# Optimization experiments

Hardware: AMD Instinct MI355X
Metric: run time of the kernel (lower is better)

The kernel has to match this reference:

```python
import jax, jax.numpy as jnp
import numpy as np

B, N, DIN, DOUT = 8, 2048, 512, 512

def setup_inputs() -> dict:
    key = jax.random.key(0)
    kx, ka, kw, kb, kattn = jax.random.split(key, 5)
    x = jax.random.normal(kx, (B, N, DIN), dtype=jnp.float32)
    adjacency_matrix = jax.random.randint(ka, (B, N, N), 0, 2, dtype=jnp.int32)
    # nn.Linear(in,out): weight [out,in], bias [out]
    lim_w = float(np.sqrt(1.0 / DIN))
    W = jax.random.uniform(kw, (DOUT, DIN), minval=-lim_w, maxval=lim_w, dtype=jnp.float32)
    b = jax.random.uniform(kb, (DOUT,), minval=-lim_w, maxval=lim_w, dtype=jnp.float32)
    # xavier_uniform for attn [out,out]
    lim_a = float(np.sqrt(6.0 / (DOUT + DOUT)))
    attn = jax.random.uniform(kattn, (DOUT, DOUT), minval=-lim_a, maxval=lim_a, dtype=jnp.float32)
    return {"x": x, "adjacency_matrix": adjacency_matrix, "W": W, "b": b, "attn": attn}

def reference(x, adjacency_matrix, W, b, attn):
    h = jnp.einsum('bni,oi->bno', x, W) + b                 # [B,N,DOUT]
    ha = jnp.einsum('bmi,ij->bmj', h, attn)                  # h @ attn
    scores = jnp.einsum('bmj,bnj->bmn', ha, h)               # bilinear pairwise scores
    scores = jnp.where(adjacency_matrix == 0, -jnp.inf, scores)
    attn_weights = jax.nn.softmax(scores, axis=-1)           # adjacency-masked softmax
    x_out = jnp.einsum('bmn,bnd->bmd', attn_weights, h)      # weighted aggregation
    return jax.nn.elu(x_out)
```

## Files before the change

kernel.cpp:

```cpp
#include <hip/hip_runtime.h>
#include <cstdint>
#include <cstddef>

typedef unsigned short u16;
using f16x8 = __attribute__((ext_vector_type(8))) _Float16;
using f32x4 = __attribute__((ext_vector_type(4))) float;
using u16x4 = __attribute__((ext_vector_type(4))) unsigned short;

__device__ __forceinline__ u16 f2h(float f) {
  union { _Float16 h; u16 u; } c;
  c.h = (_Float16)f;
  return c.u;
}

__device__ __forceinline__ void gl_lds16(const void* g, void* lds) {
  __builtin_amdgcn_global_load_lds(
      (const __attribute__((address_space(1))) void*)(uintptr_t)g,
      (__attribute__((address_space(3))) void*)(uint32_t)(uintptr_t)lds,
      16, 0, 0);
}

template <int N> __device__ __forceinline__ void vmcnt_wait() {
  if constexpr (N == 0)      asm volatile("s_waitcnt vmcnt(0)" ::: "memory");
  else if constexpr (N == 3) asm volatile("s_waitcnt vmcnt(3)" ::: "memory");
  else if constexpr (N == 4) asm volatile("s_waitcnt vmcnt(4)" ::: "memory");
  else static_assert(N == 0, "unsupported vmcnt literal");
}

__device__ __forceinline__ void block_sync() {
  asm volatile("" ::: "memory");
  __builtin_amdgcn_s_barrier();
  asm volatile("" ::: "memory");
}

template <int ROWS>
__device__ __forceinline__ void stage32(const u16* g, int ldk, u16* lds, int t) {
#pragma unroll
  for (int i = 0; i < ROWS / 128; ++i) {
    const int s   = i * 512 + t;
    const int row = s >> 2;
    const int gc  = (s & 3) ^ ((s >> 3) & 3);
    gl_lds16(g + (size_t)row * ldk + gc * 8,
             lds + (size_t)(i * 512 + (t & ~63)) * 8);
  }
}

template <int NF>
__device__ __forceinline__ void compute_tile32(
    const u16* pA, const u16* pB, f32x4 (&acc)[8][NF],
    int wm, int wn, int lm, int cq)
{
  f16x8 bf[NF];
#pragma unroll
  for (int nf = 0; nf < NF; ++nf)
    bf[nf] = *(const f16x8*)(pB + (wn + nf * 16 + lm) * 32 + cq * 8);
#pragma unroll
  for (int mf = 0; mf < 8; ++mf) {
    f16x8 a0 = *(const f16x8*)(pA + (wm + mf * 16 + lm) * 32 + cq * 8);
#pragma unroll
    for (int nf = 0; nf < NF; ++nf)
      acc[mf][nf] = __builtin_amdgcn_mfma_f32_16x16x32_f16(a0, bf[nf], acc[mf][nf], 0, 0, 0);
  }
}

template <int BN, int MODE>
__global__ __launch_bounds__(512, 2) void gemm32(
    const u16* __restrict__ A, const u16* __restrict__ Bt,
    void* __restrict__ Cv, const float* __restrict__ bias,
    int M, int Ncols, int K,
    long long strideA, long long strideB, long long strideC)
{
  constexpr int NF  = BN / 64;
  constexpr int LPT = 2 + BN / 128;

  __shared__ __align__(16) u16 sA0[256 * 32];
  __shared__ __align__(16) u16 sA1[256 * 32];
  __shared__ __align__(16) u16 sA2[256 * 32];
  __shared__ __align__(16) u16 sA3[256 * 32];
  __shared__ __align__(16) u16 sB0[BN * 32];
  __shared__ __align__(16) u16 sB1[BN * 32];
  __shared__ __align__(16) u16 sB2[BN * 32];
  __shared__ __align__(16) u16 sB3[BN * 32];

  const int bz = blockIdx.z;
  A  += (size_t)bz * strideA;
  Bt += (size_t)bz * strideB;

  const int m0 = blockIdx.y * 256;
  const int n0 = blockIdx.x * BN;
  const int t    = threadIdx.x;
  const int lane = t & 63;
  const int wave = t >> 6;
  const int wm   = (wave >> 2) * 128;
  const int wn   = (wave & 3) * (BN / 4);
  const int lm   = lane & 15;
  const int quad = lane >> 4;
  const int cq   = quad ^ ((lm >> 1) & 3);

  f32x4 acc[8][NF];
#pragma unroll
  for (int i = 0; i < 8; ++i)
#pragma unroll
    for (int j = 0; j < NF; ++j) acc[i][j] = f32x4{0.f, 0.f, 0.f, 0.f};

  const u16* Ag = A + (size_t)m0 * K;
  const u16* Bg = Bt + (size_t)n0 * K;

  const int nk = K >> 5;

  stage32<256>(Ag,      K, sA0, t);  stage32<BN>(Bg,      K, sB0, t);
  stage32<256>(Ag + 32, K, sA1, t);  stage32<BN>(Bg + 32, K, sB1, t);

  for (int kt = 0; kt < nk - 4; kt += 4) {
    vmcnt_wait<LPT>(); block_sync();
    stage32<256>(Ag + (size_t)(kt + 2) * 32, K, sA2, t);
    stage32<BN >(Bg + (size_t)(kt + 2) * 32, K, sB2, t);
    compute_tile32<NF>(sA0, sB0, acc, wm, wn, lm, cq);

    vmcnt_wait<LPT>(); block_sync();
    stage32<256>(Ag + (size_t)(kt + 3) * 32, K, sA3, t);
    stage32<BN >(Bg + (size_t)(kt + 3) * 32, K, sB3, t);
    compute_tile32<NF>(sA1, sB1, acc, wm, wn, lm, cq);

    vmcnt_wait<LPT>(); block_sync();
    stage32<256>(Ag + (size_t)(kt + 4) * 32, K, sA0, t);
    stage32<BN >(Bg + (size_t)(kt + 4) * 32, K, sB0, t);
    compute_tile32<NF>(sA2, sB2, acc, wm, wn, lm, cq);

    vmcnt_wait<LPT>(); block_sync();
    stage32<256>(Ag + (size_t)(kt + 5) * 32, K, sA1, t);
    stage32<BN >(Bg + (size_t)(kt + 5) * 32, K, sB1, t);
    compute_tile32<NF>(sA3, sB3, acc, wm, wn, lm, cq);
  }

  vmcnt_wait<LPT>(); block_sync();
  stage32<256>(Ag + (size_t)(nk - 2) * 32, K, sA2, t);
  stage32<BN >(Bg + (size_t)(nk - 2) * 32, K, sB2, t);
  compute_tile32<NF>(sA0, sB0, acc, wm, wn, lm, cq);

  vmcnt_wait<LPT>(); block_sync();
  stage32<256>(Ag + (size_t)(nk - 1) * 32, K, sA3, t);
  stage32<BN >(Bg + (size_t)(nk - 1) * 32, K, sB3, t);
  compute_tile32<NF>(sA1, sB1, acc, wm, wn, lm, cq);

  vmcnt_wait<LPT>(); block_sync();
  compute_tile32<NF>(sA2, sB2, acc, wm, wn, lm, cq);

  vmcnt_wait<0>(); block_sync();
  compute_tile32<NF>(sA3, sB3, acc, wm, wn, lm, cq);

  if (MODE == 0) {
    u16* C = (u16*)Cv + (size_t)bz * strideC;
#pragma unroll
    for (int nf = 0; nf < NF; ++nf) {
      const int col = n0 + wn + nf * 16 + lm;
      const float bv = bias ? bias[col] : 0.f;
#pragma unroll
      for (int mf = 0; mf < 8; ++mf)
#pragma unroll
        for (int r = 0; r < 4; ++r) {
          const int row = m0 + wm + mf * 16 + quad * 4 + r;
          C[(size_t)row * Ncols + col] = f2h(acc[mf][nf][r] + bv);
        }
    }
  } else {
    float* C = (float*)Cv + (size_t)bz * strideC;
#pragma unroll
    for (int nf = 0; nf < NF; ++nf) {
      const int col = n0 + wn + nf * 16 + lm;
#pragma unroll
      for (int mf = 0; mf < 8; ++mf)
#pragma unroll
        for (int r = 0; r < 4; ++r) {
          const int row = m0 + wm + mf * 16 + quad * 4 + r;
          float v = acc[mf][nf][r];
          if (MODE == 2) v = v > 0.f ? v : expm1f(v);
          C[(size_t)row * Ncols + col] = v;
        }
    }
  }
}

__global__ __launch_bounds__(256) void masked_softmax(
    const float* __restrict__ S, const int* __restrict__ adj, u16* __restrict__ P)
{
  const size_t row = blockIdx.x;
  const float* s = S + row * 2048;
  const int*   a = adj + row * 2048;
  u16*         p = P + row * 2048;
  const int t = threadIdx.x;

  float v[8];
#pragma unroll
  for (int i = 0; i < 2; ++i) {
    float4 sv = ((const float4*)s)[t + i * 256];
    int4   av = ((const int4*)a)[t + i * 256];
    v[i * 4 + 0] = av.x ? sv.x : -1e30f;
    v[i * 4 + 1] = av.y ? sv.y : -1e30f;
    v[i * 4 + 2] = av.z ? sv.z : -1e30f;
    v[i * 4 + 3] = av.w ? sv.w : -1e30f;
  }
  float mx = v[0];
#pragma unroll
  for (int i = 1; i < 8; ++i) mx = fmaxf(mx, v[i]);
#pragma unroll
  for (int o = 32; o > 0; o >>= 1) mx = fmaxf(mx, __shfl_xor(mx, o));
  __shared__ float red[4];
  if ((t & 63) == 0) red[t >> 6] = mx;
  __syncthreads();
  mx = fmaxf(fmaxf(red[0], red[1]), fmaxf(red[2], red[3]));
  __syncthreads();

  float e[8]; float sum = 0.f;
#pragma unroll
  for (int i = 0; i < 8; ++i) { e[i] = __expf(v[i] - mx); sum += e[i]; }
#pragma unroll
  for (int o = 32; o > 0; o >>= 1) sum += __shfl_xor(sum, o);
  if ((t & 63) == 0) red[t >> 6] = sum;
  __syncthreads();
  sum = red[0] + red[1] + red[2] + red[3];
  const float inv = 1.f / sum;

#pragma unroll
  for (int i = 0; i < 2; ++i) {
    u16x4 o4;
    o4[0] = f2h(e[i * 4 + 0] * inv);
    o4[1] = f2h(e[i * 4 + 1] * inv);
    o4[2] = f2h(e[i * 4 + 2] * inv);
    o4[3] = f2h(e[i * 4 + 3] * inv);
    ((u16x4*)p)[t + i * 256] = o4;
  }
}

__global__ __launch_bounds__(256) void transpose_u16(
    const u16* __restrict__ in, u16* __restrict__ outp, int R, int C)
{
  __shared__ u16 tile[64][65];
  const size_t base = (size_t)blockIdx.z * R * C;
  const int r0 = blockIdx.y * 64, c0 = blockIdx.x * 64;
  const int t = threadIdx.x;
  const int c = t & 63, rr = t >> 6;
#pragma unroll
  for (int i = 0; i < 16; ++i) {
    const int r = rr + i * 4;
    tile[r][c] = in[base + (size_t)(r0 + r) * C + c0 + c];
  }
  __syncthreads();
  const int rp = t & 63, cc = t >> 6;
#pragma unroll
  for (int i = 0; i < 16; ++i) {
    const int cq2 = cc + i * 4;
    outp[base + (size_t)(c0 + cq2) * R + r0 + rp] = tile[rp][cq2];
  }
}

__global__ __launch_bounds__(256) void cvt_f32_f16(
    const float* __restrict__ in, u16* __restrict__ outp, int n4)
{
  const int i = blockIdx.x * 256 + threadIdx.x;
  if (i >= n4) return;
  float4 v = ((const float4*)in)[i];
  u16x4 o; o[0] = f2h(v.x); o[1] = f2h(v.y); o[2] = f2h(v.z); o[3] = f2h(v.w);
  ((u16x4*)outp)[i] = o;
}

__global__ __launch_bounds__(256) void transpose_cvt(
    const float* __restrict__ in, u16* __restrict__ outp, int R, int C)
{
  const int idx = blockIdx.x * 256 + threadIdx.x;
  const int i = idx / C, j = idx % C;
  outp[(size_t)j * R + i] = f2h(in[idx]);
}

extern "C" void kernel_launch(void* const* d_in, const int* in_sizes, int n_in,
                              void* d_out, int out_size, void* d_ws, size_t ws_size,
                              hipStream_t stream) {
  (void)in_sizes; (void)n_in; (void)out_size;
  const float* x    = (const float*)d_in[0];
  const int*   adj  = (const int*)d_in[1];
  const float* W    = (const float*)d_in[2];
  const float* bvec = (const float*)d_in[3];
  const float* attn = (const float*)d_in[4];
  float* out = (float*)d_out;

  constexpr int B = 8, N = 2048, D = 512;
  constexpr size_t MN = (size_t)B * N;

  char* ws = (char*)d_ws;
  size_t off = 0;
  auto take = [&](size_t bytes) -> char* {
    char* p = ws + off;
    off += (bytes + 255) & ~(size_t)255;
    return p;
  };
  u16* xh   = (u16*)take(MN * D * 2);
  u16* Wh   = (u16*)take((size_t)D * D * 2);
  u16* attT = (u16*)take((size_t)D * D * 2);
  u16* h    = (u16*)take(MN * D * 2);
  u16* hT   = (u16*)take(MN * D * 2);
  u16* ha   = (u16*)take(MN * D * 2);

  auto al = [](size_t b) { return (b + 255) & ~(size_t)255; };
  const size_t szSf = al((size_t)B * N * N * 4), szPf = al((size_t)B * N * N * 2);
  const size_t szSb = al((size_t)N * N * 4),     szPb = al((size_t)N * N * 2);
  const bool full  = ws_size >= off + szSf + szPf;
  const bool ok_pb = ws_size >= off + szSb + szPb;
  if (!full && !ok_pb) return;

  cvt_f32_f16<<<dim3((unsigned)(MN * D / 4 / 256)), 256, 0, stream>>>(x, xh, (int)(MN * D / 4));
  cvt_f32_f16<<<dim3(D * D / 4 / 256), 256, 0, stream>>>(W, Wh, D * D / 4);
  transpose_cvt<<<dim3(D * D / 256), 256, 0, stream>>>(attn, attT, D, D);

  gemm32<128, 0><<<dim3(D / 128, MN / 256, 1), 512, 0, stream>>>(
      xh, Wh, h, bvec, (int)MN, D, D, 0, 0, 0);
  transpose_u16<<<dim3(D / 64, N / 64, B), 256, 0, stream>>>(h, hT, N, D);
  gemm32<128, 0><<<dim3(D / 128, MN / 256, 1), 512, 0, stream>>>(
      h, attT, ha, nullptr, (int)MN, D, D, 0, 0, 0);

  if (full) {
    float* S = (float*)take(szSf);
    u16*   P = (u16*)take(szPf);
    gemm32<256, 1><<<dim3(N / 256, N / 256, B), 512, 0, stream>>>(
        ha, h, S, nullptr, N, N, D,
        (long long)N * D, (long long)N * D, (long long)N * N);
    masked_softmax<<<dim3((unsigned)(B * N)), 256, 0, stream>>>(S, adj, P);
    gemm32<128, 2><<<dim3(D / 128, N / 256, B), 512, 0, stream>>>(
        P, hT, out, nullptr, N, D, N,
        (long long)N * N, (long long)D * N, (long long)N * D);
  } else {
    float* S = (float*)take(szSb);
    u16*   P = (u16*)take(szPb);
    for (int b = 0; b < B; ++b) {
      gemm32<256, 1><<<dim3(N / 256, N / 256, 1), 512, 0, stream>>>(
          ha + (size_t)b * N * D, h + (size_t)b * N * D, S, nullptr, N, N, D, 0, 0, 0);
      masked_softmax<<<dim3(N), 256, 0, stream>>>(S, adj + (size_t)b * N * N, P);
      gemm32<128, 2><<<dim3(D / 128, N / 256, 1), 512, 0, stream>>>(
          P, hT + (size_t)b * D * N, out + (size_t)b * N * D, nullptr, N, D, N, 0, 0, 0);
    }
  }
}
```

Measured before the change: 433.5 us.

## Fuse score GEMM, masked softmax and aggregation into flash-style attention kernel

Replaces the three-stage path (fp32 score GEMM to global memory, masked softmax writing fp16 probabilities, then a P·V GEMM with ELU) with one fused kernel. The fused kernel uses online softmax over 64-key tiles: K goes into LDS, Q is held in registers, and V is read directly from global memory. The goal is to drop the large B·N·N score and probability round-trips through HBM. In exchange, each 64-row query block does many block-wide syncs per tile and has low per-block tile reuse, and the grid is only 256 blocks, which may leave the GPU underoccupied.

Result: slower. 515.4 us (+18.9%).

```diff
diff --git a/kernel.cpp b/kernel.cpp
--- a/kernel.cpp
+++ b/kernel.cpp
@@ -173,62 +173,171 @@
 #pragma unroll
         for (int r = 0; r < 4; ++r) {
           const int row = m0 + wm + mf * 16 + quad * 4 + r;
-          float v = acc[mf][nf][r];
-          if (MODE == 2) v = v > 0.f ? v : expm1f(v);
-          C[(size_t)row * Ncols + col] = v;
+          C[(size_t)row * Ncols + col] = acc[mf][nf][r];
         }
     }
   }
 }
 
-__global__ __launch_bounds__(256) void masked_softmax(
-    const float* __restrict__ S, const int* __restrict__ adj, u16* __restrict__ P)
-{
-  const size_t row = blockIdx.x;
-  const float* s = S + row * 2048;
-  const int*   a = adj + row * 2048;
-  u16*         p = P + row * 2048;
+__global__ __launch_bounds__(512, 2) void fused_attn(
+    const u16* __restrict__ Qg, const u16* __restrict__ Kg,
+    const u16* __restrict__ Vt, const int* __restrict__ adj,
+    float* __restrict__ out)
+{
+  constexpr int N = 2048, D = 512;
+  __shared__ __align__(16) u16 sK[64 * 512];
+  __shared__ __align__(16) u16 sP[64 * 64];
+  __shared__ float sm[64], sl[64], sf[64];
+  __shared__ float pmx[2][64], psm[2][64];
+
+  const int bz = blockIdx.y;
+  const int q0 = blockIdx.x * 64;
+  const u16* Qb = Qg + ((size_t)bz * N + q0) * D;
+  const u16* Kb = Kg + (size_t)bz * N * D;
+  const u16* Vb = Vt + (size_t)bz * D * N;
+  const int* Ab = adj + ((size_t)bz * N + q0) * N;
+  float*     Ob = out + ((size_t)bz * N + q0) * D;
+
   const int t = threadIdx.x;
-
-  float v[8];
-#pragma unroll
-  for (int i = 0; i < 2; ++i) {
-    float4 sv = ((const float4*)s)[t + i * 256];
-    int4   av = ((const int4*)a)[t + i * 256];
-    v[i * 4 + 0] = av.x ? sv.x : -1e30f;
-    v[i * 4 + 1] = av.y ? sv.y : -1e30f;
-    v[i * 4 + 2] = av.z ? sv.z : -1e30f;
-    v[i * 4 + 3] = av.w ? sv.w : -1e30f;
-  }
-  float mx = v[0];
-#pragma unroll
-  for (int i = 1; i < 8; ++i) mx = fmaxf(mx, v[i]);
-#pragma unroll
-  for (int o = 32; o > 0; o >>= 1) mx = fmaxf(mx, __shfl_xor(mx, o));
-  __shared__ float red[4];
-  if ((t & 63) == 0) red[t >> 6] = mx;
+  const int lane = t & 63, wave = t >> 6;
+  const int lm = lane & 15, quad = lane >> 4;
+  const int qf  = wave >> 1;
+  const int kf0 = (wave & 1) * 2;
+
+  f16x8 qreg[16];
+#pragma unroll
+  for (int s = 0; s < 16; ++s)
+    qreg[s] = *(const f16x8*)(Qb + (size_t)(qf * 16 + lm) * D + s * 32 + quad * 8);
+
+  if (t < 64) { sm[t] = -1e30f; sl[t] = 0.f; }
+
+  f32x4 o_acc[4][4];
+#pragma unroll
+  for (int i = 0; i < 4; ++i)
+#pragma unroll
+    for (int j = 0; j < 4; ++j) o_acc[i][j] = f32x4{0.f, 0.f, 0.f, 0.f};
+
   __syncthreads();
-  mx = fmaxf(fmaxf(red[0], red[1]), fmaxf(red[2], red[3]));
-  __syncthreads();
-
-  float e[8]; float sum = 0.f;
-#pragma unroll
-  for (int i = 0; i < 8; ++i) { e[i] = __expf(v[i] - mx); sum += e[i]; }
-#pragma unroll
-  for (int o = 32; o > 0; o >>= 1) sum += __shfl_xor(sum, o);
-  if ((t & 63) == 0) red[t >> 6] = sum;
-  __syncthreads();
-  sum = red[0] + red[1] + red[2] + red[3];
-  const float inv = 1.f / sum;
-
-#pragma unroll
-  for (int i = 0; i < 2; ++i) {
-    u16x4 o4;
-    o4[0] = f2h(e[i * 4 + 0] * inv);
-    o4[1] = f2h(e[i * 4 + 1] * inv);
-    o4[2] = f2h(e[i * 4 + 2] * inv);
-    o4[3] = f2h(e[i * 4 + 3] * inv);
-    ((u16x4*)p)[t + i * 256] = o4;
+
+  for (int kv = 0; kv < N; kv += 64) {
+#pragma unroll
+    for (int i = 0; i < 8; ++i) {
+      const int s = i * 512 + t;
+      const int row = s >> 6, c = s & 63;
+      gl_lds16(Kb + (size_t)(kv + row) * D + (size_t)((c ^ (row & 7)) * 8),
+               sK + (size_t)(i * 512 + (t & ~63)) * 8);
+    }
+    int am[2][4];
+#pragma unroll
+    for (int j = 0; j < 2; ++j)
+#pragma unroll
+      for (int r = 0; r < 4; ++r)
+        am[j][r] = Ab[(size_t)(qf * 16 + quad * 4 + r) * N + kv + (kf0 + j) * 16 + lm];
+    f16x8 vf[4][2];
+#pragma unroll
+    for (int df = 0; df < 4; ++df)
+#pragma unroll
+      for (int ks = 0; ks < 2; ++ks)
+        vf[df][ks] = *(const f16x8*)(Vb + (size_t)(wave * 64 + df * 16 + lm) * N
+                                        + kv + ks * 32 + quad * 8);
+
+    __syncthreads();
+
+    f32x4 sfr[2];
+    sfr[0] = f32x4{0.f, 0.f, 0.f, 0.f};
+    sfr[1] = f32x4{0.f, 0.f, 0.f, 0.f};
+#pragma unroll
+    for (int j = 0; j < 2; ++j) {
+      const int krow = (kf0 + j) * 16 + lm;
+#pragma unroll
+      for (int s = 0; s < 16; ++s) {
+        f16x8 kfr = *(const f16x8*)(sK + (size_t)krow * 512
+                                       + (size_t)((((s * 4 + quad) ^ (lm & 7)) * 8)));
+        sfr[j] = __builtin_amdgcn_mfma_f32_16x16x32_f16(qreg[s], kfr, sfr[j], 0, 0, 0);
+      }
+    }
+    float vmax[4];
+#pragma unroll
+    for (int r = 0; r < 4; ++r) {
+      sfr[0][r] = am[0][r] ? sfr[0][r] : -1e30f;
+      sfr[1][r] = am[1][r] ? sfr[1][r] : -1e30f;
+      vmax[r] = fmaxf(sfr[0][r], sfr[1][r]);
+    }
+#pragma unroll
+    for (int r = 0; r < 4; ++r)
+#pragma unroll
+      for (int o = 1; o < 16; o <<= 1) vmax[r] = fmaxf(vmax[r], __shfl_xor(vmax[r], o));
+    if (lm == 0)
+#pragma unroll
+      for (int r = 0; r < 4; ++r) pmx[wave & 1][qf * 16 + quad * 4 + r] = vmax[r];
+    __syncthreads();
+
+    if (t < 64) {
+      const float mo = sm[t];
+      const float mn = fmaxf(mo, fmaxf(pmx[0][t], pmx[1][t]));
+      sm[t] = mn;
+      sf[t] = __expf(mo - mn);
+    }
+    __syncthreads();
+
+    float vsum[4];
+#pragma unroll
+    for (int r = 0; r < 4; ++r) {
+      const int row = qf * 16 + quad * 4 + r;
+      const float mn = sm[row];
+      const float e0 = __expf(sfr[0][r] - mn);
+      const float e1 = __expf(sfr[1][r] - mn);
+      vsum[r] = e0 + e1;
+      const int rq = row & 7;
+      sP[(size_t)row * 64 + (size_t)((((kf0    ) * 2 + (lm >> 3)) ^ rq) * 8) + (lm & 7)] = f2h(e0);
+      sP[(size_t)row * 64 + (size_t)((((kf0 + 1) * 2 + (lm >> 3)) ^ rq) * 8) + (lm & 7)] = f2h(e1);
+    }
+#pragma unroll
+    for (int r = 0; r < 4; ++r)
+#pragma unroll
+      for (int o = 1; o < 16; o <<= 1) vsum[r] += __shfl_xor(vsum[r], o);
+    if (lm == 0)
+#pragma unroll
+      for (int r = 0; r < 4; ++r) psm[wave & 1][qf * 16 + quad * 4 + r] = vsum[r];
+    __syncthreads();
+
+    if (t < 64) sl[t] = sl[t] * sf[t] + psm[0][t] + psm[1][t];
+
+#pragma unroll
+    for (int qi = 0; qi < 4; ++qi) {
+      float fr[4];
+#pragma unroll
+      for (int r = 0; r < 4; ++r) fr[r] = sf[qi * 16 + quad * 4 + r];
+#pragma unroll
+      for (int df = 0; df < 4; ++df)
+#pragma unroll
+        for (int r = 0; r < 4; ++r) o_acc[qi][df][r] *= fr[r];
+#pragma unroll
+      for (int ks = 0; ks < 2; ++ks) {
+        const int prow = qi * 16 + lm;
+        f16x8 pa = *(const f16x8*)(sP + (size_t)prow * 64
+                                      + (size_t)((((ks * 4 + quad) ^ (lm & 7)) * 8)));
+#pragma unroll
+        for (int df = 0; df < 4; ++df)
+          o_acc[qi][df] = __builtin_amdgcn_mfma_f32_16x16x32_f16(pa, vf[df][ks], o_acc[qi][df], 0, 0, 0);
+      }
+    }
+    __syncthreads();
+  }
+
+#pragma unroll
+  for (int qi = 0; qi < 4; ++qi) {
+    float il[4];
+#pragma unroll
+    for (int r = 0; r < 4; ++r) il[r] = 1.f / sl[qi * 16 + quad * 4 + r];
+#pragma unroll
+    for (int df = 0; df < 4; ++df)
+#pragma unroll
+      for (int r = 0; r < 4; ++r) {
+        float v = o_acc[qi][df][r] * il[r];
+        v = v > 0.f ? v : expm1f(v);
+        Ob[(size_t)(qi * 16 + quad * 4 + r) * D + wave * 64 + df * 16 + lm] = v;
+      }
   }
 }
 
@@ -299,13 +408,7 @@
   u16* h    = (u16*)take(MN * D * 2);
   u16* hT   = (u16*)take(MN * D * 2);
   u16* ha   = (u16*)take(MN * D * 2);
-
-  auto al = [](size_t b) { return (b + 255) & ~(size_t)255; };
-  const size_t szSf = al((size_t)B * N * N * 4), szPf = al((size_t)B * N * N * 2);
-  const size_t szSb = al((size_t)N * N * 4),     szPb = al((size_t)N * N * 2);
-  const bool full  = ws_size >= off + szSf + szPf;
-  const bool ok_pb = ws_size >= off + szSb + szPb;
-  if (!full && !ok_pb) return;
+  if (ws_size < off) return;
 
   cvt_f32_f16<<<dim3((unsigned)(MN * D / 4 / 256)), 256, 0, stream>>>(x, xh, (int)(MN * D / 4));
   cvt_f32_f16<<<dim3(D * D / 4 / 256), 256, 0, stream>>>(W, Wh, D * D / 4);
@@ -317,25 +420,5 @@
   gemm32<128, 0><<<dim3(D / 128, MN / 256, 1), 512, 0, stream>>>(
       h, attT, ha, nullptr, (int)MN, D, D, 0, 0, 0);
 
-  if (full) {
-    float* S = (float*)take(szSf);
-    u16*   P = (u16*)take(szPf);
-    gemm32<256, 1><<<dim3(N / 256, N / 256, B), 512, 0, stream>>>(
-        ha, h, S, nullptr, N, N, D,
-        (long long)N * D, (long long)N * D, (long long)N * N);
-    masked_softmax<<<dim3((unsigned)(B * N)), 256, 0, stream>>>(S, adj, P);
-    gemm32<128, 2><<<dim3(D / 128, N / 256, B), 512, 0, stream>>>(
-        P, hT, out, nullptr, N, D, N,
-        (long long)N * N, (long long)D * N, (long long)N * D);
-  } else {
-    float* S = (float*)take(szSb);
-    u16*   P = (u16*)take(szPb);
-    for (int b = 0; b < B; ++b) {
-      gemm32<256, 1><<<dim3(N / 256, N / 256, 1), 512, 0, stream>>>(
-          ha + (size_t)b * N * D, h + (size_t)b * N * D, S, nullptr, N, N, D, 0, 0, 0);
-      masked_softmax<<<dim3(N), 256, 0, stream>>>(S, adj + (size_t)b * N * N, P);
-      gemm32<128, 2><<<dim3(D / 128, N / 256, 1), 512, 0, stream>>>(
-          P, hT + (size_t)b * D * N, out + (size_t)b * N * D, nullptr, N, D, N, 0, 0, 0);
-    }
-  }
-}
+  fused_attn<<<dim3(N / 64, B), 512, 0, stream>>>(ha, h, hT, adj, out);
+}
```
